# Optimization experiments

Measured on AMD Instinct MI355X. Metric: run time of the kernel, lower is better.

Reference implementation:

```python
import jax, jax.numpy as jnp
import numpy as np

L, DIRS, H, I, B, T = 2, 2, 512, 1024, 64, 1024


def _gru_dir(x_seq, h0, w_ih, w_hh, b_ih, b_hh, reverse):
    """Run one GRU direction. x_seq: (B,T,in), h0: (B,H). Returns (out (B,T,H), h_T (B,H))."""
    # Precompute input projections for all timesteps: (T,B,3H)
    gi = jnp.einsum('bti,gi->tbg', x_seq, w_ih) + b_ih

    def step(h, gi_t):
        gh = h @ w_hh.T + b_hh                      # (B,3H)
        i_r, i_z, i_n = jnp.split(gi_t, 3, axis=-1)
        h_r, h_z, h_n = jnp.split(gh, 3, axis=-1)
        r = jax.nn.sigmoid(i_r + h_r)
        z = jax.nn.sigmoid(i_z + h_z)
        n = jnp.tanh(i_n + r * h_n)
        h_new = (1.0 - z) * n + z * h
        return h_new, h_new

    h_T, out = jax.lax.scan(step, h0, gi, reverse=reverse)
    return out.transpose(1, 0, 2), h_T            # (B,T,H), (B,H)


def setup_inputs() -> dict:
    key = jax.random.key(0)
    ks = jax.random.split(key, 6)
    s = 1.0 / np.sqrt(H)  # PyTorch-style init scale, avoids gate saturation
    return {
        'x':    jax.random.normal(ks[0], (B, T, I), jnp.float32),
        'h0':   jax.random.normal(ks[1], (L * DIRS, B, H), jnp.float32) * s,
        'w_ih': jax.random.normal(ks[2], (L, DIRS, 3 * H, I), jnp.float32) * s,
        'w_hh': jax.random.normal(ks[3], (L, DIRS, 3 * H, H), jnp.float32) * s,
        'b_ih': jax.random.normal(ks[4], (L, DIRS, 3 * H), jnp.float32) * s,
        'b_hh': jax.random.normal(ks[5], (L, DIRS, 3 * H), jnp.float32) * s,
    }


def reference(x, h0, w_ih, w_hh, b_ih, b_hh):
    layer_in = x
    h_finals = []
    for l in range(L):  # small fixed loop over structurally distinct layers
        out_f, hT_f = _gru_dir(layer_in, h0[2 * l],     w_ih[l, 0], w_hh[l, 0], b_ih[l, 0], b_hh[l, 0], reverse=False)
        out_b, hT_b = _gru_dir(layer_in, h0[2 * l + 1], w_ih[l, 1], w_hh[l, 1], b_ih[l, 1], b_hh[l, 1], reverse=True)
        layer_in = jnp.concatenate([out_f, out_b], axis=-1)  # (B,T,2H)
        h_finals.extend([hT_f, hT_b])
    h_n = jnp.stack(h_finals, axis=0)  # (L*2, B, H), PyTorch ordering
    return layer_in, h_n
```

## Files before the change

kernel.cpp:

```cpp
#include <hip/hip_runtime.h>
#include <stdint.h>
#include <stdio.h>

#define TL 1024
#define BB 64
#define HH 512
#define II 1024
#define NL 2
#define BT_ (BB*TL)
#define G3_ 1536
#define N2_ 3072

typedef _Float16 h8 __attribute__((ext_vector_type(8)));
typedef _Float16 h4 __attribute__((ext_vector_type(4)));
typedef _Float16 h2 __attribute__((ext_vector_type(2)));
typedef float    f4 __attribute__((ext_vector_type(4)));
typedef unsigned int u4 __attribute__((ext_vector_type(4)));
typedef unsigned int u2v __attribute__((ext_vector_type(2)));

__global__ void cvt_f2h(const float* __restrict__ src, _Float16* __restrict__ dst, size_t n4) {
  size_t i = (size_t)blockIdx.x*blockDim.x + threadIdx.x;
  size_t stride = (size_t)gridDim.x*blockDim.x;
  for (; i < n4; i += stride) {
    f4 v = ((const f4*)src)[i];
    h4 o;
    o[0] = (_Float16)v[0]; o[1] = (_Float16)v[1];
    o[2] = (_Float16)v[2]; o[3] = (_Float16)v[3];
    ((h4*)dst)[i] = o;
  }
}

#define LDA 40
__launch_bounds__(256)
__global__ void gemm_gi(const _Float16* __restrict__ A, const _Float16* __restrict__ Bw,
                        const float* __restrict__ bias, _Float16* __restrict__ gi)
{
  const int bn = blockIdx.x, bm = blockIdx.y;
  const int tid = threadIdx.x;
  const int wave = tid >> 6, lane = tid & 63;
  const int wm = wave >> 1, wn = wave & 1;
  const int lo = lane & 15, hi = lane >> 4;
  __shared__ _Float16 As[128*LDA];
  __shared__ _Float16 Bs[128*LDA];
  f4 acc[4][4] = {};
  const int r0 = tid >> 2, c0 = (tid & 3)*8;
  const _Float16* Ag = A + (size_t)(bm*128)*II;
  const _Float16* Bg = Bw + (size_t)(bn*128)*II;
  u4 a0 = *(const u4*)(Ag + (size_t)r0*II + c0);
  u4 a1 = *(const u4*)(Ag + (size_t)(64+r0)*II + c0);
  u4 b0 = *(const u4*)(Bg + (size_t)r0*II + c0);
  u4 b1 = *(const u4*)(Bg + (size_t)(64+r0)*II + c0);
  for (int kt = 0; kt < 32; ++kt) {
    __syncthreads();
    *(u4*)&As[r0*LDA + c0] = a0;
    *(u4*)&As[(64+r0)*LDA + c0] = a1;
    *(u4*)&Bs[r0*LDA + c0] = b0;
    *(u4*)&Bs[(64+r0)*LDA + c0] = b1;
    if (kt+1 < 32) {
      const int off = (kt+1)*32 + c0;
      a0 = *(const u4*)(Ag + (size_t)r0*II + off);
      a1 = *(const u4*)(Ag + (size_t)(64+r0)*II + off);
      b0 = *(const u4*)(Bg + (size_t)r0*II + off);
      b1 = *(const u4*)(Bg + (size_t)(64+r0)*II + off);
    }
    __syncthreads();
    h8 af[4], bf[4];
    #pragma unroll
    for (int i = 0; i < 4; ++i)
      af[i] = *(const h8*)&As[(wm*64 + i*16 + lo)*LDA + hi*8];
    #pragma unroll
    for (int j = 0; j < 4; ++j)
      bf[j] = *(const h8*)&Bs[(wn*64 + j*16 + lo)*LDA + hi*8];
    #pragma unroll
    for (int i = 0; i < 4; ++i)
      #pragma unroll
      for (int j = 0; j < 4; ++j)
        acc[i][j] = __builtin_amdgcn_mfma_f32_16x16x32_f16(af[i], bf[j], acc[i][j], 0, 0, 0);
  }
  const int nbase = bn*128 + wn*64;
  const int mbase = bm*128 + wm*64;
  #pragma unroll
  for (int j = 0; j < 4; ++j) {
    int n = nbase + j*16 + lo;
    int dir = (n >= G3_) ? 1 : 0;
    int row = n - dir*G3_;
    float bs = bias[n];
    #pragma unroll
    for (int i = 0; i < 4; ++i) {
      int m0 = mbase + i*16 + hi*4;
      #pragma unroll
      for (int v = 0; v < 4; ++v)
        gi[((size_t)dir*BT_ + (size_t)(m0+v))*G3_ + row] = (_Float16)(acc[i][j][v] + bs);
    }
  }
}

#define LDW 520
__launch_bounds__(384, 1)
__global__ void gru_layer(const _Float16* __restrict__ gi,
                          const _Float16* __restrict__ whh,
                          const float* __restrict__ bhh,
                          const float* __restrict__ h0,
                          unsigned long long* __restrict__ tagh,
                          _Float16* __restrict__ out_mid,
                          float* __restrict__ out_fin,
                          float* __restrict__ hn_out,
                          int layer)
{
  const int bid = blockIdx.x;
  const int gg = bid & 7, d = gg & 1, g = gg >> 1;
  const int member = bid >> 3;
  const int j0 = member * 32, b0 = g * 16;
  const int tid = threadIdx.x;
  const int wave = tid >> 6, lane = tid & 63, lo = lane & 15, hi = lane >> 4;
  const int gate = wave >> 1, jh = wave & 1;

  __shared__ _Float16 wlds[3][32][LDW];
  __shared__ _Float16 hlds[16][LDW];
  __shared__ float    ghlds[3][32][17];
  __shared__ unsigned wok[8];

  const _Float16* wsrc = whh + (size_t)d*G3_*HH;
  #pragma unroll
  for (int it = 0; it < 16; ++it) {
    int idx = it*384 + tid;
    int row = idx >> 6;
    int c8 = (idx & 63) * 8;
    int gt = row >> 5, jj = row & 31;
    u4 v = *(const u4*)(wsrc + (size_t)(gt*HH + j0 + jj)*HH + c8);
    *(u4*)&wlds[gt][jj][c8] = v;
  }

  const int ejp = tid & 15;
  const int eb  = tid >> 4;
  const bool ew = (tid < 256);
  const int ejA = j0 + 2*ejp;

  unsigned long long* Tb = tagh + (size_t)d*2*BB*256;

  float hj[2];
  float bhr[2], bhz[2], bhn[2];

  if (ew) {
    #pragma unroll
    for (int u = 0; u < 2; ++u) {
      bhr[u] = bhh[(size_t)d*G3_ + 0*HH + ejA + u];
      bhz[u] = bhh[(size_t)d*G3_ + 1*HH + ejA + u];
      bhn[u] = bhh[(size_t)d*G3_ + 2*HH + ejA + u];
      hj[u]  = h0[((size_t)(2*layer + d)*BB + b0 + eb)*HH + ejA + u];
    }
    h2 p; p[0] = (_Float16)hj[0]; p[1] = (_Float16)hj[1];
    unsigned long long ent = (unsigned long long)__builtin_bit_cast(unsigned, p) | (1ull << 32);
    unsigned long long* ptr = Tb + (size_t)0*BB*256 + (size_t)(b0 + eb)*256 + (member*16 + ejp);
    __hip_atomic_store(ptr, ent, __ATOMIC_RELAXED, __HIP_MEMORY_SCOPE_AGENT);
  }
  __syncthreads();

  for (int s = 0; s < TL; ++s) {
    const int t = d ? (TL-1 - s) : s;
    const int rpar = s & 1, wpar = rpar ^ 1;
    const unsigned tgt = (unsigned)(s + 1);
    unsigned giR = 0, giZ = 0, giN = 0;
    if (ew) {
      const _Float16* p = gi + ((size_t)d*BT_ + (size_t)(b0 + eb)*TL + t)*(size_t)G3_ + ejA;
      giR = *(const unsigned*)(p);
      giZ = *(const unsigned*)(p + HH);
      giN = *(const unsigned*)(p + 2*HH);
    }
    {
      const unsigned long long* Trd = Tb + (size_t)rpar*BB*256;
      for (;;) {
        unsigned long long E0[6], E1[6];
        #pragma unroll
        for (int it = 0; it < 6; ++it) {
          int idx = it*384 + tid;
          if (idx < 2048) {
            const unsigned long long* pa = Trd + (size_t)(b0 + (idx >> 7))*256 + (idx & 127)*2;
            E0[it] = __hip_atomic_load(pa,     __ATOMIC_RELAXED, __HIP_MEMORY_SCOPE_AGENT);
            E1[it] = __hip_atomic_load(pa + 1, __ATOMIC_RELAXED, __HIP_MEMORY_SCOPE_AGENT);
          }
        }
        unsigned okm = 1u;
        #pragma unroll
        for (int it = 0; it < 6; ++it) {
          int idx = it*384 + tid;
          if (idx < 2048) {
            okm &= (unsigned)((E0[it] >> 32) >= tgt) & (unsigned)((E1[it] >> 32) >= tgt);
            int b = idx >> 7, j4 = (idx & 127)*4;
            u2v dv; dv[0] = (unsigned)E0[it]; dv[1] = (unsigned)E1[it];
            *(u2v*)&hlds[b][j4] = dv;
          }
        }
        unsigned long long bal = __ballot(okm != 0u);
        if (lane == 0) wok[wave] = (bal == ~0ull) ? 1u : 0u;
        __syncthreads();
        unsigned allok = wok[0] & wok[1] & wok[2] & wok[3] & wok[4] & wok[5];
        if (allok) break;
        __syncthreads();
      }
    }
    f4 acc = {0.f, 0.f, 0.f, 0.f};
    #pragma unroll
    for (int kk = 0; kk < 16; ++kk) {
      h8 af = *(const h8*)&hlds[lo][kk*32 + hi*8];
      h8 bf = *(const h8*)&wlds[gate][jh*16 + lo][kk*32 + hi*8];
      acc = __builtin_amdgcn_mfma_f32_16x16x32_f16(af, bf, acc, 0, 0, 0);
    }
    #pragma unroll
    for (int v = 0; v < 4; ++v)
      ghlds[gate][jh*16 + lo][hi*4 + v] = acc[v];
    __syncthreads();
    if (ew) {
      h2 pR = __builtin_bit_cast(h2, giR);
      h2 pZ = __builtin_bit_cast(h2, giZ);
      h2 pN = __builtin_bit_cast(h2, giN);
      h2 hnew; float hv[2];
      #pragma unroll
      for (int u = 0; u < 2; ++u) {
        float ir = (float)pR[u], iz = (float)pZ[u], inn = (float)pN[u];
        float hr = ghlds[0][2*ejp+u][eb] + bhr[u];
        float hz = ghlds[1][2*ejp+u][eb] + bhz[u];
        float hn = ghlds[2][2*ejp+u][eb] + bhn[u];
        float rr = 1.f/(1.f + __expf(-(ir + hr)));
        float zz = 1.f/(1.f + __expf(-(iz + hz)));
        float xx = inn + rr*hn;
        float nn = 1.f - 2.f/(__expf(2.f*xx) + 1.f);
        float h  = (1.f - zz)*nn + zz*hj[u];
        hj[u] = h; hnew[u] = (_Float16)h; hv[u] = h;
      }
      unsigned hu = __builtin_bit_cast(unsigned, hnew);
      unsigned long long ent = (unsigned long long)hu | ((unsigned long long)(s + 2) << 32);
      unsigned long long* ptr = Tb + (size_t)wpar*BB*256 + (size_t)(b0 + eb)*256 + (member*16 + ejp);
      __hip_atomic_store(ptr, ent, __ATOMIC_RELAXED, __HIP_MEMORY_SCOPE_AGENT);
      if (out_mid) {
        *(unsigned*)(out_mid + ((size_t)(b0+eb)*TL + t)*(size_t)(2*HH) + d*HH + ejA) = hu;
      } else {
        u2v ov; ov[0] = __builtin_bit_cast(unsigned, hv[0]); ov[1] = __builtin_bit_cast(unsigned, hv[1]);
        *(u2v*)(out_fin + ((size_t)(b0+eb)*TL + t)*(size_t)(2*HH) + d*HH + ejA) = ov;
      }
    }
  }
  if (ew) {
    #pragma unroll
    for (int u = 0; u < 2; ++u)
      hn_out[((size_t)(2*layer + d)*BB + b0 + eb)*HH + ejA + u] = hj[u];
  }
}

extern "C" void kernel_launch(void* const* d_in, const int* in_sizes, int n_in,
                              void* d_out, int out_size, void* d_ws, size_t ws_size,
                              hipStream_t stream) {
  (void)in_sizes; (void)n_in; (void)out_size;
  const float* x   = (const float*)d_in[0];
  const float* h0  = (const float*)d_in[1];
  const float* wih = (const float*)d_in[2];
  const float* whh = (const float*)d_in[3];
  const float* bih = (const float*)d_in[4];
  const float* bhh = (const float*)d_in[5];
  float* out = (float*)d_out;

  char* ws = (char*)d_ws;
  size_t off = 0;
  auto alloc = [&](size_t bytes) {
    char* p = ws + off;
    off += (bytes + 255) & ~(size_t)255;
    return p;
  };
  _Float16* x16   = (_Float16*)alloc((size_t)BT_*II*2);
  _Float16* mid16 = (_Float16*)alloc((size_t)BT_*II*2);
  _Float16* gi16  = (_Float16*)alloc((size_t)2*BT_*G3_*2);
  _Float16* wih16 = (_Float16*)alloc((size_t)NL*N2_*II*2);
  _Float16* whh16 = (_Float16*)alloc((size_t)NL*N2_*HH*2);
  unsigned long long* tagh = (unsigned long long*)alloc((size_t)NL*2*2*BB*256*8);
  if (off > ws_size) {
    fprintf(stderr, "kernel_launch: workspace too small: need %zu have %zu\n", off, ws_size);
    return;
  }

  hipMemsetAsync(tagh, 0, (size_t)NL*2*2*BB*256*8, stream);
  cvt_f2h<<<2048, 256, 0, stream>>>(x,   x16,   (size_t)BT_*II/4);
  cvt_f2h<<<512,  256, 0, stream>>>(wih, wih16, (size_t)NL*N2_*II/4);
  cvt_f2h<<<512,  256, 0, stream>>>(whh, whh16, (size_t)NL*N2_*HH/4);

  float* hn = out + (size_t)BT_*II;

  gemm_gi<<<dim3(24, 512), 256, 0, stream>>>(x16, wih16, bih, gi16);
  gru_layer<<<128, 384, 0, stream>>>(gi16, whh16, bhh, h0, tagh,
                                     mid16, nullptr, hn, 0);
  gemm_gi<<<dim3(24, 512), 256, 0, stream>>>(mid16, wih16 + (size_t)N2_*II, bih + N2_, gi16);
  gru_layer<<<128, 384, 0, stream>>>(gi16, whh16 + (size_t)N2_*HH, bhh + N2_, h0,
                                     tagh + (size_t)2*2*BB*256, nullptr, out, hn, 1);
}
```

Measured before the change: 8.284 ms.

## Pipeline hidden-state polling in K-quarters overlapped with MFMA

Replaces the block-wide poll-all-then-barrier loop with per-thread polling of four K-quarter chunks of the hidden-state tag buffer. Only the 256 elementwise threads load, and each keeps spinning on just its own quarter. Each quarter is written to LDS and then consumed by its four MFMA steps after a lightweight barrier. The aim is to start the matmul on h columns from producers that finished early and to drop the ballot/wok reduction and double syncthreads per retry. The cost is more barriers per step and reliance on per-thread spin correctness, with raw s_barrier and waitcnt used for ordering.

```diff
diff --git a/kernel.cpp b/kernel.cpp
--- a/kernel.cpp
+++ b/kernel.cpp
@@ -118,7 +118,6 @@
   __shared__ _Float16 wlds[3][32][LDW];
   __shared__ _Float16 hlds[16][LDW];
   __shared__ float    ghlds[3][32][17];
-  __shared__ unsigned wok[8];
 
   const _Float16* wsrc = whh + (size_t)d*G3_*HH;
   #pragma unroll
@@ -160,51 +159,59 @@
     const int t = d ? (TL-1 - s) : s;
     const int rpar = s & 1, wpar = rpar ^ 1;
     const unsigned tgt = (unsigned)(s + 1);
+    const unsigned long long* Trd = Tb + (size_t)rpar*BB*256;
     unsigned giR = 0, giZ = 0, giN = 0;
+    unsigned long long E[16];
     if (ew) {
       const _Float16* p = gi + ((size_t)d*BT_ + (size_t)(b0 + eb)*TL + t)*(size_t)G3_ + ejA;
       giR = *(const unsigned*)(p);
       giZ = *(const unsigned*)(p + HH);
       giN = *(const unsigned*)(p + 2*HH);
-    }
-    {
-      const unsigned long long* Trd = Tb + (size_t)rpar*BB*256;
-      for (;;) {
-        unsigned long long E0[6], E1[6];
+      #pragma unroll
+      for (int q = 0; q < 4; ++q)
         #pragma unroll
-        for (int it = 0; it < 6; ++it) {
-          int idx = it*384 + tid;
-          if (idx < 2048) {
-            const unsigned long long* pa = Trd + (size_t)(b0 + (idx >> 7))*256 + (idx & 127)*2;
-            E0[it] = __hip_atomic_load(pa,     __ATOMIC_RELAXED, __HIP_MEMORY_SCOPE_AGENT);
-            E1[it] = __hip_atomic_load(pa + 1, __ATOMIC_RELAXED, __HIP_MEMORY_SCOPE_AGENT);
+        for (int k = 0; k < 4; ++k) {
+          int i = tid*2 + (k >> 1);
+          E[q*4+k] = __hip_atomic_load(
+              Trd + (size_t)(b0 + (i >> 5))*256 + q*64 + (i & 31)*2 + (k & 1),
+              __ATOMIC_RELAXED, __HIP_MEMORY_SCOPE_AGENT);
+        }
+    }
+    f4 acc = {0.f, 0.f, 0.f, 0.f};
+    #pragma unroll
+    for (int q = 0; q < 4; ++q) {
+      if (ew) {
+        for (;;) {
+          unsigned ok = 1u;
+          #pragma unroll
+          for (int k = 0; k < 4; ++k)
+            ok &= (unsigned)((E[q*4+k] >> 32) >= tgt);
+          if (ok) break;
+          #pragma unroll
+          for (int k = 0; k < 4; ++k) {
+            int i = tid*2 + (k >> 1);
+            E[q*4+k] = __hip_atomic_load(
+                Trd + (size_t)(b0 + (i >> 5))*256 + q*64 + (i & 31)*2 + (k & 1),
+                __ATOMIC_RELAXED, __HIP_MEMORY_SCOPE_AGENT);
           }
         }
-        unsigned okm = 1u;
         #pragma unroll
-        for (int it = 0; it < 6; ++it) {
-          int idx = it*384 + tid;
-          if (idx < 2048) {
-            okm &= (unsigned)((E0[it] >> 32) >= tgt) & (unsigned)((E1[it] >> 32) >= tgt);
-            int b = idx >> 7, j4 = (idx & 127)*4;
-            u2v dv; dv[0] = (unsigned)E0[it]; dv[1] = (unsigned)E1[it];
-            *(u2v*)&hlds[b][j4] = dv;
-          }
+        for (int k = 0; k < 2; ++k) {
+          int i = tid*2 + k;
+          int b = i >> 5, p = i & 31;
+          u2v dv; dv[0] = (unsigned)E[q*4 + k*2]; dv[1] = (unsigned)E[q*4 + k*2 + 1];
+          *(u2v*)&hlds[b][q*128 + p*4] = dv;
         }
-        unsigned long long bal = __ballot(okm != 0u);
-        if (lane == 0) wok[wave] = (bal == ~0ull) ? 1u : 0u;
-        __syncthreads();
-        unsigned allok = wok[0] & wok[1] & wok[2] & wok[3] & wok[4] & wok[5];
-        if (allok) break;
-        __syncthreads();
       }
-    }
-    f4 acc = {0.f, 0.f, 0.f, 0.f};
-    #pragma unroll
-    for (int kk = 0; kk < 16; ++kk) {
-      h8 af = *(const h8*)&hlds[lo][kk*32 + hi*8];
-      h8 bf = *(const h8*)&wlds[gate][jh*16 + lo][kk*32 + hi*8];
-      acc = __builtin_amdgcn_mfma_f32_16x16x32_f16(af, bf, acc, 0, 0, 0);
+      asm volatile("s_waitcnt lgkmcnt(0)" ::: "memory");
+      __builtin_amdgcn_s_barrier();
+      __builtin_amdgcn_sched_barrier(0);
+      #pragma unroll
+      for (int kk = q*4; kk < q*4 + 4; ++kk) {
+        h8 af = *(const h8*)&hlds[lo][kk*32 + hi*8];
+        h8 bf = *(const h8*)&wlds[gate][jh*16 + lo][kk*32 + hi*8];
+        acc = __builtin_amdgcn_mfma_f32_16x16x32_f16(af, bf, acc, 0, 0, 0);
+      }
     }
     #pragma unroll
     for (int v = 0; v < 4; ++v)
```

Result: faster. 7.194 ms (median of 2 runs) (-13.2%).

## Replace tagged hidden-state polling with per-block flags and prefetch gate inputs

Applied to the files above, without the earlier changes.

Switches the inter-block hidden-state exchange from 64-bit tagged entries, which every thread polled until all tags matched, to plain 32-bit values plus a per-member flag array. One wave spins on 16 flags and the whole block then reads the exchanged hidden state once. Each block writes its values with atomic exchanges, waits for them to finish (vmcnt), and then publishes its step flag. The next step's input-projection values are also prefetched after the flag store so their load latency overlaps the wait. This halves exchange traffic and drops the repeated polling loads. In exchange it relies on relaxed atomics and vmcnt waits for ordering, which risks memory-ordering bugs.

```diff
diff --git a/kernel.cpp b/kernel.cpp
--- a/kernel.cpp
+++ b/kernel.cpp
@@ -101,7 +101,8 @@
                           const _Float16* __restrict__ whh,
                           const float* __restrict__ bhh,
                           const float* __restrict__ h0,
-                          unsigned long long* __restrict__ tagh,
+                          unsigned* __restrict__ hexch,
+                          unsigned* __restrict__ flags,
                           _Float16* __restrict__ out_mid,
                           float* __restrict__ out_fin,
                           float* __restrict__ hn_out,
@@ -118,7 +119,6 @@
   __shared__ _Float16 wlds[3][32][LDW];
   __shared__ _Float16 hlds[16][LDW];
   __shared__ float    ghlds[3][32][17];
-  __shared__ unsigned wok[8];
 
   const _Float16* wsrc = whh + (size_t)d*G3_*HH;
   #pragma unroll
@@ -136,10 +136,11 @@
   const bool ew = (tid < 256);
   const int ejA = j0 + 2*ejp;
 
-  unsigned long long* Tb = tagh + (size_t)d*2*BB*256;
+  unsigned* FL = flags + gg*16;
 
   float hj[2];
   float bhr[2], bhz[2], bhn[2];
+  unsigned gR = 0, gZ = 0, gN = 0;
 
   if (ew) {
     #pragma unroll
@@ -150,55 +151,55 @@
       hj[u]  = h0[((size_t)(2*layer + d)*BB + b0 + eb)*HH + ejA + u];
     }
     h2 p; p[0] = (_Float16)hj[0]; p[1] = (_Float16)hj[1];
-    unsigned long long ent = (unsigned long long)__builtin_bit_cast(unsigned, p) | (1ull << 32);
-    unsigned long long* ptr = Tb + (size_t)0*BB*256 + (size_t)(b0 + eb)*256 + (member*16 + ejp);
-    __hip_atomic_store(ptr, ent, __ATOMIC_RELAXED, __HIP_MEMORY_SCOPE_AGENT);
-  }
+    unsigned pu = __builtin_bit_cast(unsigned, p);
+    unsigned* ptr = hexch + ((size_t)(0*2 + 0)*0  , ((size_t)(d*2 + 0)*BB + b0 + eb)*256 + member*16 + ejp);
+    unsigned old = __hip_atomic_exchange(ptr, pu, __ATOMIC_RELAXED, __HIP_MEMORY_SCOPE_AGENT);
+    asm volatile("" :: "v"(old));
+    const int t0 = d ? (TL-1) : 0;
+    const _Float16* pg = gi + ((size_t)d*BT_ + (size_t)(b0 + eb)*TL + t0)*(size_t)G3_ + ejA;
+    gR = *(const unsigned*)(pg);
+    gZ = *(const unsigned*)(pg + HH);
+    gN = *(const unsigned*)(pg + 2*HH);
+  }
+  asm volatile("s_waitcnt vmcnt(0)" ::: "memory");
   __syncthreads();
+  if (tid == 0)
+    __hip_atomic_store(&FL[member], 1u, __ATOMIC_RELAXED, __HIP_MEMORY_SCOPE_AGENT);
 
   for (int s = 0; s < TL; ++s) {
     const int t = d ? (TL-1 - s) : s;
     const int rpar = s & 1, wpar = rpar ^ 1;
     const unsigned tgt = (unsigned)(s + 1);
-    unsigned giR = 0, giZ = 0, giN = 0;
+
+    if (wave == 4) {
+      const int m = lane & 15;
+      const bool act = (lane < 16) && (m != member);
+      for (;;) {
+        unsigned v = tgt;
+        if (act) v = __hip_atomic_load(&FL[m], __ATOMIC_RELAXED, __HIP_MEMORY_SCOPE_AGENT);
+        if (__ballot(v >= tgt) == ~0ull) break;
+      }
+    }
+    __builtin_amdgcn_s_barrier();
+    __builtin_amdgcn_sched_barrier(0);
     if (ew) {
-      const _Float16* p = gi + ((size_t)d*BT_ + (size_t)(b0 + eb)*TL + t)*(size_t)G3_ + ejA;
-      giR = *(const unsigned*)(p);
-      giZ = *(const unsigned*)(p + HH);
-      giN = *(const unsigned*)(p + 2*HH);
-    }
-    {
-      const unsigned long long* Trd = Tb + (size_t)rpar*BB*256;
-      for (;;) {
-        unsigned long long E0[6], E1[6];
-        #pragma unroll
-        for (int it = 0; it < 6; ++it) {
-          int idx = it*384 + tid;
-          if (idx < 2048) {
-            const unsigned long long* pa = Trd + (size_t)(b0 + (idx >> 7))*256 + (idx & 127)*2;
-            E0[it] = __hip_atomic_load(pa,     __ATOMIC_RELAXED, __HIP_MEMORY_SCOPE_AGENT);
-            E1[it] = __hip_atomic_load(pa + 1, __ATOMIC_RELAXED, __HIP_MEMORY_SCOPE_AGENT);
-          }
-        }
-        unsigned okm = 1u;
-        #pragma unroll
-        for (int it = 0; it < 6; ++it) {
-          int idx = it*384 + tid;
-          if (idx < 2048) {
-            okm &= (unsigned)((E0[it] >> 32) >= tgt) & (unsigned)((E1[it] >> 32) >= tgt);
-            int b = idx >> 7, j4 = (idx & 127)*4;
-            u2v dv; dv[0] = (unsigned)E0[it]; dv[1] = (unsigned)E1[it];
-            *(u2v*)&hlds[b][j4] = dv;
-          }
-        }
-        unsigned long long bal = __ballot(okm != 0u);
-        if (lane == 0) wok[wave] = (bal == ~0ull) ? 1u : 0u;
-        __syncthreads();
-        unsigned allok = wok[0] & wok[1] & wok[2] & wok[3] & wok[4] & wok[5];
-        if (allok) break;
-        __syncthreads();
+      const unsigned long long* src = (const unsigned long long*)hexch
+          + (((size_t)(d*2 + rpar)*BB + b0 + eb)*256)/2 + ejp*8;
+      unsigned long long Ev[8];
+      #pragma unroll
+      for (int k = 0; k < 8; ++k)
+        Ev[k] = __hip_atomic_load(src + k, __ATOMIC_RELAXED, __HIP_MEMORY_SCOPE_AGENT);
+      #pragma unroll
+      for (int k2 = 0; k2 < 4; ++k2) {
+        u4 v;
+        v[0] = (unsigned)Ev[2*k2];     v[1] = (unsigned)(Ev[2*k2] >> 32);
+        v[2] = (unsigned)Ev[2*k2 + 1]; v[3] = (unsigned)(Ev[2*k2 + 1] >> 32);
+        *(u4*)&hlds[eb][ejp*32 + k2*8] = v;
       }
     }
+    asm volatile("s_waitcnt lgkmcnt(0)" ::: "memory");
+    __builtin_amdgcn_s_barrier();
+    __builtin_amdgcn_sched_barrier(0);
     f4 acc = {0.f, 0.f, 0.f, 0.f};
     #pragma unroll
     for (int kk = 0; kk < 16; ++kk) {
@@ -209,11 +210,13 @@
     #pragma unroll
     for (int v = 0; v < 4; ++v)
       ghlds[gate][jh*16 + lo][hi*4 + v] = acc[v];
-    __syncthreads();
+    asm volatile("s_waitcnt lgkmcnt(0)" ::: "memory");
+    __builtin_amdgcn_s_barrier();
+    __builtin_amdgcn_sched_barrier(0);
     if (ew) {
-      h2 pR = __builtin_bit_cast(h2, giR);
-      h2 pZ = __builtin_bit_cast(h2, giZ);
-      h2 pN = __builtin_bit_cast(h2, giN);
+      h2 pR = __builtin_bit_cast(h2, gR);
+      h2 pZ = __builtin_bit_cast(h2, gZ);
+      h2 pN = __builtin_bit_cast(h2, gN);
       h2 hnew; float hv[2];
       #pragma unroll
       for (int u = 0; u < 2; ++u) {
@@ -229,15 +232,28 @@
         hj[u] = h; hnew[u] = (_Float16)h; hv[u] = h;
       }
       unsigned hu = __builtin_bit_cast(unsigned, hnew);
-      unsigned long long ent = (unsigned long long)hu | ((unsigned long long)(s + 2) << 32);
-      unsigned long long* ptr = Tb + (size_t)wpar*BB*256 + (size_t)(b0 + eb)*256 + (member*16 + ejp);
-      __hip_atomic_store(ptr, ent, __ATOMIC_RELAXED, __HIP_MEMORY_SCOPE_AGENT);
+      unsigned* ptr = hexch + ((size_t)(d*2 + wpar)*BB + b0 + eb)*256 + member*16 + ejp;
+      unsigned old = __hip_atomic_exchange(ptr, hu, __ATOMIC_RELAXED, __HIP_MEMORY_SCOPE_AGENT);
+      asm volatile("" :: "v"(old));
       if (out_mid) {
         *(unsigned*)(out_mid + ((size_t)(b0+eb)*TL + t)*(size_t)(2*HH) + d*HH + ejA) = hu;
       } else {
         u2v ov; ov[0] = __builtin_bit_cast(unsigned, hv[0]); ov[1] = __builtin_bit_cast(unsigned, hv[1]);
         *(u2v*)(out_fin + ((size_t)(b0+eb)*TL + t)*(size_t)(2*HH) + d*HH + ejA) = ov;
       }
+    }
+    asm volatile("s_waitcnt vmcnt(0)" ::: "memory");
+    __builtin_amdgcn_s_barrier();
+    __builtin_amdgcn_sched_barrier(0);
+    if (tid == 0)
+      __hip_atomic_store(&FL[member], (unsigned)(s + 2), __ATOMIC_RELAXED, __HIP_MEMORY_SCOPE_AGENT);
+    if (ew) {
+      int sn = (s + 1 < TL) ? s + 1 : s;
+      int tn = d ? (TL-1 - sn) : sn;
+      const _Float16* pg = gi + ((size_t)d*BT_ + (size_t)(b0 + eb)*TL + tn)*(size_t)G3_ + ejA;
+      gR = *(const unsigned*)(pg);
+      gZ = *(const unsigned*)(pg + HH);
+      gN = *(const unsigned*)(pg + 2*HH);
     }
   }
   if (ew) {
@@ -271,13 +287,14 @@
   _Float16* gi16  = (_Float16*)alloc((size_t)2*BT_*G3_*2);
   _Float16* wih16 = (_Float16*)alloc((size_t)NL*N2_*II*2);
   _Float16* whh16 = (_Float16*)alloc((size_t)NL*N2_*HH*2);
-  unsigned long long* tagh = (unsigned long long*)alloc((size_t)NL*2*2*BB*256*8);
+  unsigned* hexch = (unsigned*)alloc((size_t)NL*2*2*BB*256*4);
+  unsigned* flags = (unsigned*)alloc((size_t)NL*8*16*4);
   if (off > ws_size) {
     fprintf(stderr, "kernel_launch: workspace too small: need %zu have %zu\n", off, ws_size);
     return;
   }
 
-  hipMemsetAsync(tagh, 0, (size_t)NL*2*2*BB*256*8, stream);
+  hipMemsetAsync(flags, 0, (size_t)NL*8*16*4, stream);
   cvt_f2h<<<2048, 256, 0, stream>>>(x,   x16,   (size_t)BT_*II/4);
   cvt_f2h<<<512,  256, 0, stream>>>(wih, wih16, (size_t)NL*N2_*II/4);
   cvt_f2h<<<512,  256, 0, stream>>>(whh, whh16, (size_t)NL*N2_*HH/4);
@@ -285,9 +302,10 @@
   float* hn = out + (size_t)BT_*II;
 
   gemm_gi<<<dim3(24, 512), 256, 0, stream>>>(x16, wih16, bih, gi16);
-  gru_layer<<<128, 384, 0, stream>>>(gi16, whh16, bhh, h0, tagh,
+  gru_layer<<<128, 384, 0, stream>>>(gi16, whh16, bhh, h0, hexch, flags,
                                      mid16, nullptr, hn, 0);
   gemm_gi<<<dim3(24, 512), 256, 0, stream>>>(mid16, wih16 + (size_t)N2_*II, bih + N2_, gi16);
   gru_layer<<<128, 384, 0, stream>>>(gi16, whh16 + (size_t)N2_*HH, bhh + N2_, h0,
-                                     tagh + (size_t)2*2*BB*256, nullptr, out, hn, 1);
+                                     hexch + (size_t)2*2*BB*256, flags + 8*16,
+                                     nullptr, out, hn, 1);
 }
```

Measured after the change: 8.122 ms. 2.0% less time.
